# Performance work log

Measured on AMD Instinct MI355X. Metric: run time of the kernel, lower is better.

Reference implementation:

```python
import jax, jax.numpy as jnp
import numpy as np

L, D, H, DFF, A, S = 8, 1024, 16, 4096, 4096, 66
T = S + 1  # 67 after pool token
DK = D // H
EPS = 1e-5


def _pos_enc(t, d):
    pos = np.arange(t, dtype=np.float32)[:, None]
    div = np.exp(np.arange(0, d, 2, dtype=np.float32) * (-np.log(10000.0) / d))
    pe = np.zeros((t, d), dtype=np.float32)
    pe[:, 0::2] = np.sin(pos * div)
    pe[:, 1::2] = np.cos(pos * div)
    return jnp.asarray(pe)


def _ln(x, g, b):
    m = jnp.mean(x, axis=-1, keepdims=True)
    v = jnp.mean(jnp.square(x - m), axis=-1, keepdims=True)
    return (x - m) * jax.lax.rsqrt(v + EPS) * g + b


def setup_inputs() -> dict:
    key = jax.random.key(0)
    ks = jax.random.split(key, 12)
    B = 256
    sc = 0.02
    return {
        "x": jax.random.randint(ks[0], (B, S), 0, A, dtype=jnp.int32),
        "emb": jax.random.normal(ks[1], (A, D), jnp.float32) * sc,
        "pool": jax.random.normal(ks[2], (D,), jnp.float32) * sc,
        "Wq": jax.random.normal(ks[3], (L, D, D), jnp.float32) * sc,
        "Wk": jax.random.normal(ks[4], (L, D, D), jnp.float32) * sc,
        "Wv": jax.random.normal(ks[5], (L, D, D), jnp.float32) * sc,
        "Wo": jax.random.normal(ks[6], (L, D, D), jnp.float32) * sc,
        "rel_bias": jax.random.normal(ks[7], (L, H, 78, 78), jnp.float32) * sc,
        "ln1_g": jnp.ones((L, D), jnp.float32),
        "ln1_b": jnp.zeros((L, D), jnp.float32),
        "ln2_g": jnp.ones((L, D), jnp.float32),
        "ln2_b": jnp.zeros((L, D), jnp.float32),
        "W1": jax.random.normal(ks[8], (L, D, DFF), jnp.float32) * sc,
        "b1": jnp.zeros((L, DFF), jnp.float32),
        "W2": jax.random.normal(ks[9], (L, DFF, D), jnp.float32) * sc,
        "b2": jnp.zeros((L, D), jnp.float32),
        "Wout": jax.random.normal(ks[10], (D, A), jnp.float32) * sc,
        "bout": jnp.zeros((A,), jnp.float32),
    }


def reference(x, emb, pool, Wq, Wk, Wv, Wo, rel_bias, ln1_g, ln1_b, ln2_g, ln2_b,
              W1, b1, W2, b2, Wout, bout):
    B = x.shape[0]
    h = emb[x] * jnp.sqrt(jnp.float32(D))            # (B, S, D)
    h = jnp.concatenate([jnp.broadcast_to(pool, (B, 1, D)), h], axis=1)  # (B, T, D)
    h = h + _pos_enc(T, D)[None]
    scale = 1.0 / jnp.sqrt(jnp.float32(DK))
    for i in range(L):
        q = (h @ Wq[i]).reshape(B, T, H, DK)
        k = (h @ Wk[i]).reshape(B, T, H, DK)
        v = (h @ Wv[i]).reshape(B, T, H, DK)
        scores = jnp.einsum("bqhd,bkhd->bhqk", q, k) * scale + rel_bias[i][:, :T, :T]
        attn = jax.nn.softmax(scores, axis=-1)
        ctx = jnp.einsum("bhqk,bkhd->bqhd", attn, v).reshape(B, T, D)
        h = _ln(h + ctx @ Wo[i], ln1_g[i], ln1_b[i])
        f = jax.nn.gelu(h @ W1[i] + b1[i], approximate=False) @ W2[i] + b2[i]
        h = _ln(h + f, ln2_g[i], ln2_b[i])
    return h[:, 0, :] @ Wout + bout  # (B, A)
```

## Files before the change

kernel.cpp:

```cpp
#include <hip/hip_runtime.h>
#include <math.h>

typedef unsigned short u16;
typedef __attribute__((ext_vector_type(8))) short short8;
typedef __attribute__((ext_vector_type(4))) float f32x4;

#define LAYERS 8
#define D 1024
#define NH 16
#define DKH 64
#define DFF 4096
#define SEQ 66
#define TT 67
#define BATCH 256
#define ROWS (BATCH*TT)
#define VOCAB 4096
#define TP 80
#define KP 96
#define QS 3072

__device__ __forceinline__ float bf2f(u16 v){
  unsigned int u = ((unsigned int)v) << 16;
  return __builtin_bit_cast(float, u);
}
__device__ __forceinline__ u16 f2bf(float f){
  unsigned int u = __builtin_bit_cast(unsigned int, f);
  u += 0x7FFFu + ((u >> 16) & 1u);
  return (u16)(u >> 16);
}
__device__ __forceinline__ void gload16(const u16* g, u16* l){
  __builtin_amdgcn_global_load_lds((const __attribute__((address_space(1))) void*)g,
                                   (__attribute__((address_space(3))) void*)l, 16, 0, 0);
}

__device__ __forceinline__ void tc_tile(const float* __restrict__ src, u16* __restrict__ dst,
                                        int R, int C, int bx, int by, int tx, int ty){
  __shared__ float tile[32][33];
  const int c0 = bx * 32, r0 = by * 32;
  #pragma unroll
  for (int i = 0; i < 32; i += 8)
    tile[ty + i][tx] = src[(size_t)(r0 + ty + i) * C + (c0 + tx)];
  __syncthreads();
  #pragma unroll
  for (int i = 0; i < 32; i += 8)
    dst[(size_t)(c0 + ty + i) * R + (r0 + tx)] = f2bf(tile[tx][ty + i]);
}

__global__ void transpose6(const float* __restrict__ Wq, const float* __restrict__ Wk,
                           const float* __restrict__ Wv, const float* __restrict__ Wo,
                           const float* __restrict__ W1, const float* __restrict__ W2,
                           u16* __restrict__ WqkvT, u16* __restrict__ WoT,
                           u16* __restrict__ W1T, u16* __restrict__ W2T){
  const int tx = threadIdx.x, ty = threadIdx.y;
  int b = blockIdx.x;
  if (b < 4096){
    const int which = b >> 10, idx = b & 1023;
    const float* s = which == 0 ? Wq : which == 1 ? Wk : which == 2 ? Wv : Wo;
    u16* d = which == 3 ? WoT : WqkvT + which * D * D;
    tc_tile(s, d, D, D, idx & 31, idx >> 5, tx, ty);
  } else if (b < 8192){
    const int idx = b - 4096;
    tc_tile(W1, W1T, D, DFF, idx & 127, idx >> 7, tx, ty);
  } else {
    const int idx = b - 8192;
    tc_tile(W2, W2T, DFF, D, idx & 31, idx >> 5, tx, ty);
  }
}

__global__ void transpose_cast(const float* __restrict__ src, u16* __restrict__ dst,
                               int R, int C){
  tc_tile(src, dst, R, C, blockIdx.x, blockIdx.y, threadIdx.x, threadIdx.y);
}

__global__ void embed_kernel(const int* __restrict__ x, const float* __restrict__ emb,
                             const float* __restrict__ pool, u16* __restrict__ hb){
  const int row = blockIdx.x;
  const int b = row / TT, t = row % TT;
  const int d0 = threadIdx.x * 4;
  float v[4];
  if (t == 0){
    const float4 p4 = *(const float4*)&pool[d0];
    v[0] = p4.x; v[1] = p4.y; v[2] = p4.z; v[3] = p4.w;
  } else {
    const int id = x[b * SEQ + (t - 1)];
    const float4 e4 = *(const float4*)&emb[(size_t)id * D + d0];
    v[0] = e4.x * 32.f; v[1] = e4.y * 32.f; v[2] = e4.z * 32.f; v[3] = e4.w * 32.f;
  }
  const float c = -logf(10000.f) / (float)D;
  float o[4];
  #pragma unroll
  for (int j = 0; j < 4; j++){
    const int d = d0 + j;
    const int p = d >> 1;
    const float freq = expf((float)(2 * p) * c);
    const float ang = (float)t * freq;
    const float pe = (d & 1) ? cosf(ang) : sinf(ang);
    o[j] = v[j] + pe;
  }
  const unsigned int lo = (unsigned)f2bf(o[0]) | ((unsigned)f2bf(o[1]) << 16);
  const unsigned int hi = (unsigned)f2bf(o[2]) | ((unsigned)f2bf(o[3]) << 16);
  *(uint2*)&hb[(size_t)row * D + d0] = make_uint2(lo, hi);
}

__global__ void ln_kernel(u16* __restrict__ hio, const u16* __restrict__ res,
                          const float* __restrict__ g, const float* __restrict__ bta){
  const int row = blockIdx.x;
  const int tid = threadIdx.x;
  const size_t off = (size_t)row * D + tid * 4;
  const uint2 a2 = *(const uint2*)&hio[off];
  const uint2 r2 = *(const uint2*)&res[off];
  const float s0 = bf2f((u16)(a2.x & 0xffff)) + bf2f((u16)(r2.x & 0xffff));
  const float s1 = bf2f((u16)(a2.x >> 16))    + bf2f((u16)(r2.x >> 16));
  const float s2 = bf2f((u16)(a2.y & 0xffff)) + bf2f((u16)(r2.y & 0xffff));
  const float s3 = bf2f((u16)(a2.y >> 16))    + bf2f((u16)(r2.y >> 16));
  float sum = s0 + s1 + s2 + s3;
  float sq = s0*s0 + s1*s1 + s2*s2 + s3*s3;
  #pragma unroll
  for (int m = 32; m >= 1; m >>= 1){ sum += __shfl_xor(sum, m); sq += __shfl_xor(sq, m); }
  __shared__ float red[2][4];
  const int w = tid >> 6;
  if ((tid & 63) == 0){ red[0][w] = sum; red[1][w] = sq; }
  __syncthreads();
  sum = red[0][0] + red[0][1] + red[0][2] + red[0][3];
  sq  = red[1][0] + red[1][1] + red[1][2] + red[1][3];
  const float mean = sum * (1.f / D);
  const float var = sq * (1.f / D) - mean * mean;
  const float rs = rsqrtf(var + 1e-5f);
  const float4 gv = *(const float4*)&g[tid * 4];
  const float4 bv = *(const float4*)&bta[tid * 4];
  const float o0 = (s0 - mean) * rs * gv.x + bv.x;
  const float o1 = (s1 - mean) * rs * gv.y + bv.y;
  const float o2 = (s2 - mean) * rs * gv.z + bv.z;
  const float o3 = (s3 - mean) * rs * gv.w + bv.w;
  const unsigned int lo = (unsigned)f2bf(o0) | ((unsigned)f2bf(o1) << 16);
  const unsigned int hi = (unsigned)f2bf(o2) | ((unsigned)f2bf(o3) << 16);
  *(uint2*)&hio[off] = make_uint2(lo, hi);
}

__global__ __launch_bounds__(256) void attn_kernel(const u16* __restrict__ qkv,
    const float* __restrict__ rel, u16* __restrict__ ctxb){
  __shared__ u16 Qf[8 * 81 * 8];
  __shared__ u16 Kf[8 * 81 * 8];
  __shared__ u16 Vf[12 * 65 * 8];
  __shared__ u16 Pf[12 * 81 * 8];
  __shared__ float Ss[TP][84];
  const int bh = blockIdx.x;
  const int b = bh >> 4, hh = bh & 15;
  const int tid = threadIdx.x, w = tid >> 6, l = tid & 63;
  const size_t qvbase = (size_t)(b * TT) * QS + hh * DKH;
  const size_t obase  = (size_t)(b * TT) * D + hh * DKH;

  {
    const int r0 = tid >> 4, c4 = (tid & 15) * 4;
    const int g = c4 >> 3, e = c4 & 7;
    for (int r = r0; r < TP; r += 16){
      uint2 q2 = make_uint2(0u, 0u), k2 = make_uint2(0u, 0u);
      if (r < TT){
        q2 = *(const uint2*)&qkv[qvbase + (size_t)r * QS + c4];
        k2 = *(const uint2*)&qkv[qvbase + 1024 + (size_t)r * QS + c4];
      }
      *(uint2*)&Qf[(g * 81 + r) * 8 + e] = q2;
      *(uint2*)&Kf[(g * 81 + r) * 8 + e] = k2;
    }
    for (int j = r0; j < KP; j += 16){
      u16 v4[4] = {0, 0, 0, 0};
      if (j < TT) *(uint2*)v4 = *(const uint2*)&qkv[qvbase + 2048 + (size_t)j * QS + c4];
      const int gg = j >> 3, ee = j & 7;
      #pragma unroll
      for (int d = 0; d < 4; d++)
        Vf[(gg * 65 + (c4 + d)) * 8 + ee] = v4[d];
    }
  }
  __syncthreads();

  const int fr = l & 15, gg = l >> 4;
  for (int p = w; p < 25; p += 4){
    const int rt = p / 5, ct = p % 5;
    f32x4 acc = {};
    #pragma unroll
    for (int kk = 0; kk < 2; kk++){
      const short8 a  = *(const short8*)&Qf[((kk * 4 + gg) * 81 + rt * 16 + fr) * 8];
      const short8 bf = *(const short8*)&Kf[((kk * 4 + gg) * 81 + ct * 16 + fr) * 8];
      acc = __builtin_amdgcn_mfma_f32_16x16x32_bf16(a, bf, acc, 0, 0, 0);
    }
    const int col = ct * 16 + fr;
    #pragma unroll
    for (int r = 0; r < 4; r++){
      const int row = rt * 16 + gg * 4 + r;
      float sv = -1e30f;
      if (row < TT && col < TT)
        sv = acc[r] * 0.125f + rel[((size_t)hh * 78 + row) * 78 + col];
      Ss[row][col] = sv;
    }
  }
  __syncthreads();

  for (int row = w; row < TP; row += 4){
    const float s1 = Ss[row][l];
    const float s2 = (l < 16) ? Ss[row][64 + l] : -1e30f;
    float mx = fmaxf(s1, s2);
    #pragma unroll
    for (int m = 32; m >= 1; m >>= 1) mx = fmaxf(mx, __shfl_xor(mx, m));
    const float e1 = __expf(s1 - mx);
    const float e2 = (l < 16) ? __expf(s2 - mx) : 0.f;
    float sum = e1 + e2;
    #pragma unroll
    for (int m = 32; m >= 1; m >>= 1) sum += __shfl_xor(sum, m);
    const float inv = 1.f / sum;
    Pf[((l >> 3) * 81 + row) * 8 + (l & 7)] = f2bf(e1 * inv);
    if (l < 16){
      Pf[((8  + (l >> 3)) * 81 + row) * 8 + (l & 7)] = f2bf(e2 * inv);
      Pf[((10 + (l >> 3)) * 81 + row) * 8 + (l & 7)] = 0;
    }
  }
  __syncthreads();

  for (int p = w; p < 20; p += 4){
    const int rt = p >> 2, ct = p & 3;
    f32x4 acc = {};
    #pragma unroll
    for (int kk = 0; kk < 3; kk++){
      const short8 a  = *(const short8*)&Pf[((kk * 4 + gg) * 81 + rt * 16 + fr) * 8];
      const short8 bf = *(const short8*)&Vf[((kk * 4 + gg) * 65 + ct * 16 + fr) * 8];
      acc = __builtin_amdgcn_mfma_f32_16x16x32_bf16(a, bf, acc, 0, 0, 0);
    }
    #pragma unroll
    for (int r = 0; r < 4; r++){
      const int row = rt * 16 + gg * 4 + r;
      if (row < TT)
        ctxb[obase + (size_t)row * D + ct * 16 + fr] = f2bf(acc[r]);
    }
  }
}

template<int OBF16, int BIAS, int GELU>
__global__ __launch_bounds__(256, 4) void gemm_bt(
    const u16* __restrict__ A, int lda,
    const u16* __restrict__ Bt,
    void* __restrict__ Cv, int ldc,
    const float* __restrict__ bias, int K, int nby)
{
  __shared__ u16 As[2][128 * 32];
  __shared__ u16 Bs[2][128 * 32];
  const int nwg = gridDim.x, bid = blockIdx.x;
  const int q8 = nwg >> 3, r8 = nwg & 7;
  const int xcd = bid & 7, off = bid >> 3;
  const int wg = (xcd < r8 ? xcd * (q8 + 1) : r8 * (q8 + 1) + (xcd - r8) * q8) + off;
  const int m0 = (wg / nby) * 128, n0 = (wg % nby) * 128;

  const int tid = threadIdx.x;
  const int l = tid & 63, w = tid >> 6;
  const int wr = w >> 1, wc = w & 1;
  f32x4 acc[4][4] = {};
  const int lr = l >> 2;
  const int lseg = ((l & 3) ^ ((l >> 3) & 3)) * 8;
  const u16* ga0 = A + (size_t)(m0 + w * 32 + lr) * lda + lseg;
  const u16* ga1 = A + (size_t)(m0 + w * 32 + 16 + lr) * lda + lseg;
  const u16* gb0 = Bt + (size_t)(n0 + w * 32 + lr) * K + lseg;
  const u16* gb1 = Bt + (size_t)(n0 + w * 32 + 16 + lr) * K + lseg;
  const int fr = l & 15;
  const int kg = ((l >> 4) ^ ((l >> 1) & 3)) * 8;

#define STAGE(sel, kc) do { \
    gload16(ga0 + (kc), &As[sel][(w * 32) * 32]); \
    gload16(ga1 + (kc), &As[sel][(w * 32 + 16) * 32]); \
    gload16(gb0 + (kc), &Bs[sel][(w * 32) * 32]); \
    gload16(gb1 + (kc), &Bs[sel][(w * 32 + 16) * 32]); \
  } while (0)

  const int nkt = K >> 5;
  STAGE(0, 0);
  __syncthreads();
  int cur = 0;
  #pragma unroll 1
  for (int kt = 0; kt < nkt; ++kt){
    if (kt + 1 < nkt) STAGE(cur ^ 1, (kt + 1) * 32);
    short8 af[4], bf[4];
    #pragma unroll
    for (int i = 0; i < 4; i++){
      af[i] = *(const short8*)&As[cur][(wr * 64 + i * 16 + fr) * 32 + kg];
      bf[i] = *(const short8*)&Bs[cur][(wc * 64 + i * 16 + fr) * 32 + kg];
    }
    #pragma unroll
    for (int i = 0; i < 4; i++)
      #pragma unroll
      for (int j = 0; j < 4; j++)
        acc[i][j] = __builtin_amdgcn_mfma_f32_16x16x32_bf16(af[i], bf[j], acc[i][j], 0, 0, 0);
    __syncthreads();
    cur ^= 1;
  }
#undef STAGE

  const int rg = (l >> 4) * 4;
  #pragma unroll
  for (int i = 0; i < 4; i++){
    #pragma unroll
    for (int j = 0; j < 4; j++){
      const int col = n0 + wc * 64 + j * 16 + fr;
      const float bv = BIAS ? bias[col] : 0.f;
      #pragma unroll
      for (int r = 0; r < 4; r++){
        const int row = m0 + wr * 64 + i * 16 + rg + r;
        float xv = acc[i][j][r] + bv;
        if (GELU) xv = 0.5f * xv * (1.f + erff(xv * 0.70710678118f));
        if (OBF16) ((u16*)Cv)[(size_t)row * ldc + col] = f2bf(xv);
        else       ((float*)Cv)[(size_t)row * ldc + col] = xv;
      }
    }
  }
}

extern "C" void kernel_launch(void* const* d_in, const int* in_sizes, int n_in,
                              void* d_out, int out_size, void* d_ws, size_t ws_size,
                              hipStream_t stream) {
  const int*   x       = (const int*)  d_in[0];
  const float* emb     = (const float*)d_in[1];
  const float* pool    = (const float*)d_in[2];
  const float* Wq      = (const float*)d_in[3];
  const float* Wk      = (const float*)d_in[4];
  const float* Wv      = (const float*)d_in[5];
  const float* Wo      = (const float*)d_in[6];
  const float* rel     = (const float*)d_in[7];
  const float* ln1_g   = (const float*)d_in[8];
  const float* ln1_b   = (const float*)d_in[9];
  const float* ln2_g   = (const float*)d_in[10];
  const float* ln2_b   = (const float*)d_in[11];
  const float* W1      = (const float*)d_in[12];
  const float* b1      = (const float*)d_in[13];
  const float* W2      = (const float*)d_in[14];
  const float* b2      = (const float*)d_in[15];
  const float* Wout    = (const float*)d_in[16];
  const float* bout    = (const float*)d_in[17];
  float* out = (float*)d_out;

  const size_t SZ_WDD  = (size_t)D * D * 2;
  const size_t SZ_WDF  = (size_t)D * DFF * 2;
  const size_t SZ_HB   = (size_t)ROWS * D * 2;
  const size_t need = 4*SZ_WDD + 3*SZ_WDF + 6*SZ_HB;
  if (ws_size < need) return;

  char* p = (char*)d_ws;
  u16* WqkvT = (u16*)p; p += 3*SZ_WDD;
  u16* WoT   = (u16*)p; p += SZ_WDD;
  u16* W1T   = (u16*)p; p += SZ_WDF;
  u16* W2T   = (u16*)p; p += SZ_WDF;
  u16* WouT  = (u16*)p; p += SZ_WDF;
  u16* hb    = (u16*)p; p += SZ_HB;
  u16* qkv   = (u16*)p; p += 3*SZ_HB;
  u16* ctxb  = (u16*)p; p += SZ_HB;
  u16* gb    = qkv;
  u16* tmpb  = (u16*)p; p += SZ_HB;

  dim3 tb(32, 8);
  transpose_cast<<<dim3(VOCAB/32, D/32), tb, 0, stream>>>(Wout, WouT, D, VOCAB);
  embed_kernel<<<ROWS, 256, 0, stream>>>(x, emb, pool, hb);

  const int MB = ROWS / 128;
  for (int l = 0; l < LAYERS; ++l){
    const size_t wo = (size_t)l * D * D;
    const size_t wf = (size_t)l * D * DFF;
    transpose6<<<12288, tb, 0, stream>>>(Wq + wo, Wk + wo, Wv + wo, Wo + wo,
                                         W1 + wf, W2 + wf, WqkvT, WoT, W1T, W2T);

    gemm_bt<1,0,0><<<MB * (QS/128),  256, 0, stream>>>(hb, D, WqkvT, qkv, QS, nullptr, D, QS/128);
    attn_kernel<<<BATCH*NH, 256, 0, stream>>>(qkv, rel + (size_t)l*NH*78*78, ctxb);
    gemm_bt<1,0,0><<<MB * (D/128),   256, 0, stream>>>(ctxb, D, WoT, tmpb, D, nullptr, D, D/128);
    ln_kernel<<<ROWS, 256, 0, stream>>>(hb, tmpb, ln1_g + l*D, ln1_b + l*D);
    gemm_bt<1,1,1><<<MB * (DFF/128), 256, 0, stream>>>(hb, D, W1T, gb, DFF, b1 + l*DFF, D, DFF/128);
    gemm_bt<1,1,0><<<MB * (D/128),   256, 0, stream>>>(gb, DFF, W2T, tmpb, D, b2 + l*D, DFF, D/128);
    ln_kernel<<<ROWS, 256, 0, stream>>>(hb, tmpb, ln2_g + l*D, ln2_b + l*D);
  }
  gemm_bt<0,1,0><<<(BATCH/128) * (VOCAB/128), 256, 0, stream>>>(
      hb, TT * D, WouT, out, VOCAB, bout, D, VOCAB/128);
}
```

Measured before the change: 6.269 ms.

## Add 8-wave 128x128 GEMM variant for FFN layers and raise occupancy hint

Adds a gemm_w kernel that computes the same 128x128 tile with 512 threads (8 waves, 2x4 wave grid), so each wave holds a 64x32 accumulator instead of 64x64. Each wave loads 16 rows of A and B per stage, and A fragments are loaded per row-tile inside the MFMA loop. The FFN up and down projections now use this kernel. The existing gemm_bt launch bound is raised from 4 to 5 blocks per CU. The intent is more waves in flight to hide LDS and global latency, at the cost of less register-level reuse per wave, and the tighter bounds could force register spills.

```diff
diff --git a/kernel.cpp b/kernel.cpp
--- a/kernel.cpp
+++ b/kernel.cpp
@@ -234,7 +234,7 @@
 }
 
 template<int OBF16, int BIAS, int GELU>
-__global__ __launch_bounds__(256, 4) void gemm_bt(
+__global__ __launch_bounds__(256, 5) void gemm_bt(
     const u16* __restrict__ A, int lda,
     const u16* __restrict__ Bt,
     void* __restrict__ Cv, int ldc,
@@ -297,6 +297,78 @@
     #pragma unroll
     for (int j = 0; j < 4; j++){
       const int col = n0 + wc * 64 + j * 16 + fr;
+      const float bv = BIAS ? bias[col] : 0.f;
+      #pragma unroll
+      for (int r = 0; r < 4; r++){
+        const int row = m0 + wr * 64 + i * 16 + rg + r;
+        float xv = acc[i][j][r] + bv;
+        if (GELU) xv = 0.5f * xv * (1.f + erff(xv * 0.70710678118f));
+        if (OBF16) ((u16*)Cv)[(size_t)row * ldc + col] = f2bf(xv);
+        else       ((float*)Cv)[(size_t)row * ldc + col] = xv;
+      }
+    }
+  }
+}
+
+template<int OBF16, int BIAS, int GELU>
+__global__ __launch_bounds__(512, 8) void gemm_w(
+    const u16* __restrict__ A, int lda,
+    const u16* __restrict__ Bt,
+    void* __restrict__ Cv, int ldc,
+    const float* __restrict__ bias, int K, int nby)
+{
+  __shared__ u16 As[2][128 * 32];
+  __shared__ u16 Bs[2][128 * 32];
+  const int nwg = gridDim.x, bid = blockIdx.x;
+  const int q8 = nwg >> 3, r8 = nwg & 7;
+  const int xcd = bid & 7, off = bid >> 3;
+  const int wg = (xcd < r8 ? xcd * (q8 + 1) : r8 * (q8 + 1) + (xcd - r8) * q8) + off;
+  const int m0 = (wg / nby) * 128, n0 = (wg % nby) * 128;
+
+  const int tid = threadIdx.x;
+  const int l = tid & 63, w = tid >> 6;
+  const int wr = w >> 2, wc = w & 3;
+  f32x4 acc[4][2] = {};
+  const int lr = l >> 2;
+  const int lseg = ((l & 3) ^ ((l >> 3) & 3)) * 8;
+  const u16* ga0 = A + (size_t)(m0 + w * 16 + lr) * lda + lseg;
+  const u16* gb0 = Bt + (size_t)(n0 + w * 16 + lr) * K + lseg;
+  const int fr = l & 15;
+  const int kg = ((l >> 4) ^ ((l >> 1) & 3)) * 8;
+
+#define STAGEW(sel, kc) do { \
+    gload16(ga0 + (kc), &As[sel][(w * 16) * 32]); \
+    gload16(gb0 + (kc), &Bs[sel][(w * 16) * 32]); \
+  } while (0)
+
+  const int nkt = K >> 5;
+  STAGEW(0, 0);
+  __syncthreads();
+  int cur = 0;
+  #pragma unroll 1
+  for (int kt = 0; kt < nkt; ++kt){
+    if (kt + 1 < nkt) STAGEW(cur ^ 1, (kt + 1) * 32);
+    short8 bf[2];
+    #pragma unroll
+    for (int j = 0; j < 2; j++)
+      bf[j] = *(const short8*)&Bs[cur][(wc * 32 + j * 16 + fr) * 32 + kg];
+    #pragma unroll
+    for (int i = 0; i < 4; i++){
+      const short8 ai = *(const short8*)&As[cur][(wr * 64 + i * 16 + fr) * 32 + kg];
+      acc[i][0] = __builtin_amdgcn_mfma_f32_16x16x32_bf16(ai, bf[0], acc[i][0], 0, 0, 0);
+      acc[i][1] = __builtin_amdgcn_mfma_f32_16x16x32_bf16(ai, bf[1], acc[i][1], 0, 0, 0);
+    }
+    __syncthreads();
+    cur ^= 1;
+  }
+#undef STAGEW
+
+  const int rg = (l >> 4) * 4;
+  #pragma unroll
+  for (int i = 0; i < 4; i++){
+    #pragma unroll
+    for (int j = 0; j < 2; j++){
+      const int col = n0 + wc * 32 + j * 16 + fr;
       const float bv = BIAS ? bias[col] : 0.f;
       #pragma unroll
       for (int r = 0; r < 4; r++){
@@ -366,8 +438,8 @@
     attn_kernel<<<BATCH*NH, 256, 0, stream>>>(qkv, rel + (size_t)l*NH*78*78, ctxb);
     gemm_bt<1,0,0><<<MB * (D/128),   256, 0, stream>>>(ctxb, D, WoT, tmpb, D, nullptr, D, D/128);
     ln_kernel<<<ROWS, 256, 0, stream>>>(hb, tmpb, ln1_g + l*D, ln1_b + l*D);
-    gemm_bt<1,1,1><<<MB * (DFF/128), 256, 0, stream>>>(hb, D, W1T, gb, DFF, b1 + l*DFF, D, DFF/128);
-    gemm_bt<1,1,0><<<MB * (D/128),   256, 0, stream>>>(gb, DFF, W2T, tmpb, D, b2 + l*D, DFF, D/128);
+    gemm_w<1,1,1><<<MB * (DFF/128),  512, 0, stream>>>(hb, D, W1T, gb, DFF, b1 + l*DFF, D, DFF/128);
+    gemm_w<1,1,0><<<MB * (D/128),    512, 0, stream>>>(gb, DFF, W2T, tmpb, D, b2 + l*D, DFF, D/128);
     ln_kernel<<<ROWS, 256, 0, stream>>>(hb, tmpb, ln2_g + l*D, ln2_b + l*D);
   }
   gemm_bt<0,1,0><<<(BATCH/128) * (VOCAB/128), 256, 0, stream>>>(
```

Result: slower. 6.685 ms (+6.6%).
